# Kernel optimization log

Hardware: AMD Instinct MI355X
Metric: run time of the kernel (lower is better)

Reference implementation:

```python
import jax, jax.numpy as jnp
import numpy as np

N_NODES = 100000
N_EDGES = 800000
D_FEAT = 64
N_HIDDEN = 64
N_CLASSES = 16


def setup_inputs() -> dict:
    key = jax.random.key(0)
    ks = jax.random.split(key, 10)
    s = 1.0 / np.sqrt(N_HIDDEN)
    inp = {
        "x": jax.random.normal(ks[0], (N_NODES, D_FEAT), dtype=jnp.float32),
        "edge_index": jax.random.randint(ks[1], (2, N_EDGES), 0, N_NODES, dtype=jnp.int64)
        if jax.config.jax_enable_x64 else jax.random.randint(ks[1], (2, N_EDGES), 0, N_NODES, dtype=jnp.int32),
        "W1": jax.random.normal(ks[2], (D_FEAT, N_HIDDEN), dtype=jnp.float32) * s,
        "b1": jnp.zeros((N_HIDDEN,), jnp.float32),
        "W2": jax.random.normal(ks[3], (N_HIDDEN, N_HIDDEN), dtype=jnp.float32) * s,
        "b2": jnp.zeros((N_HIDDEN,), jnp.float32),
        "W3": jax.random.normal(ks[4], (N_HIDDEN, N_HIDDEN), dtype=jnp.float32) * s,
        "b3": jnp.zeros((N_HIDDEN,), jnp.float32),
        "Wf1": jax.random.normal(ks[5], (N_HIDDEN, N_HIDDEN), dtype=jnp.float32) * s,
        "bf1": jnp.zeros((N_HIDDEN,), jnp.float32),
        "Wf2": jax.random.normal(ks[6], (N_HIDDEN, N_HIDDEN), dtype=jnp.float32) * s,
        "bf2": jnp.zeros((N_HIDDEN,), jnp.float32),
        "Wf3": jax.random.normal(ks[7], (N_HIDDEN, N_CLASSES), dtype=jnp.float32) * s,
        "bf3": jnp.zeros((N_CLASSES,), jnp.float32),
    }
    return inp


def reference(x, edge_index, W1, b1, W2, b2, W3, b3, Wf1, bf1, Wf2, bf2, Wf3, bf3):
    N = x.shape[0]
    loops = jnp.arange(N, dtype=edge_index.dtype)
    src = jnp.concatenate([edge_index[0], loops])  # [E+N]
    dst = jnp.concatenate([edge_index[1], loops])
    # symmetric GCN normalization with self-loops (edge weight 1)
    deg = jax.ops.segment_sum(jnp.ones(src.shape[0], x.dtype), dst, num_segments=N)
    dis = jax.lax.rsqrt(jnp.maximum(deg, 1.0))  # deg >= 1 due to self-loops
    norm = dis[src] * dis[dst]  # [E+N]

    def gcn(h, W, b):
        h = h @ W  # [N, H]
        msg = h[src] * norm[:, None]  # [E+N, H] gather
        return jax.ops.segment_sum(msg, dst, num_segments=N) + b  # scatter-add

    y = jax.nn.relu(gcn(x, W1, b1))
    y = jax.nn.relu(gcn(y, W2, b2))
    y = jax.nn.relu(gcn(y, W3, b3))
    y = jax.nn.relu(y @ Wf1 + bf1)
    y = jax.nn.relu(y @ Wf2 + bf2)
    y = y @ Wf3 + bf3
    return jax.nn.log_softmax(y, axis=1)
```

## Files before the change

kernel.cpp:

```cpp
#include <hip/hip_runtime.h>
#include <hip/hip_bf16.h>

#define NN 100000
#define NE 800000
#define EBLK 391
#define NBUK 196
#define BSTRIDE 6144

typedef __attribute__((ext_vector_type(8))) short bf16x8;
typedef __attribute__((ext_vector_type(4))) float f32x4;

__device__ __forceinline__ unsigned short f2b(float f) {
  unsigned int x = __float_as_uint(f);
  return (unsigned short)((x + 0x7fffu + ((x >> 16) & 1u)) >> 16);
}
__device__ __forceinline__ float b2f(short us) {
  return __uint_as_float(((unsigned int)(unsigned short)us) << 16);
}
__device__ __forceinline__ void acc8(float* acc, bf16x8 v) {
#pragma unroll
  for (int i = 0; i < 8; ++i) acc[i] += b2f(v[i]);
}

static __global__ __launch_bounds__(256) void k_scatter(const int* __restrict__ src, const int* __restrict__ dst,
                                                        int* __restrict__ gcur, int* __restrict__ ebuf) {
  __shared__ int hist[256];
  __shared__ int lstart[256];
  __shared__ int gbase[256];
  __shared__ int cur[NBUK];
  __shared__ int2 sbuf[2048];
  int tid = threadIdx.x, blk = blockIdx.x;
  hist[tid] = 0;
  __syncthreads();
  int base = blk * 2048;
  int dd[8], ss[8];
#pragma unroll
  for (int i = 0; i < 8; ++i) {
    int e = base + tid + 256 * i;
    if (e < NE) {
      dd[i] = dst[e]; ss[i] = src[e];
      atomicAdd(&hist[dd[i] >> 9], 1);
    } else dd[i] = -1;
  }
  __syncthreads();
  int v = hist[tid];
  lstart[tid] = v;
  __syncthreads();
  for (int off = 1; off < 256; off <<= 1) {
    int t = (tid >= off) ? lstart[tid - off] : 0;
    __syncthreads();
    lstart[tid] += t;
    __syncthreads();
  }
  int excl = lstart[tid] - v;
  __syncthreads();
  lstart[tid] = excl;
  if (tid < NBUK) {
    cur[tid] = 0;
    gbase[tid] = (v > 0) ? atomicAdd(&gcur[tid], v) : 0;
  }
  __syncthreads();
#pragma unroll
  for (int i = 0; i < 8; ++i) {
    if (dd[i] >= 0) {
      int b = dd[i] >> 9;
      int p = atomicAdd(&cur[b], 1);
      sbuf[lstart[b] + p] = make_int2((ss[i] << 9) | (dd[i] & 511), b);
    }
  }
  __syncthreads();
  int m = NE - base; if (m > 2048) m = 2048;
#pragma unroll
  for (int i = 0; i < 8; ++i) {
    int j = tid + 256 * i;
    if (j < m) {
      int2 e = sbuf[j];
      int b = e.y;
      int gpos = b * BSTRIDE + gbase[b] + (j - lstart[b]);
      ebuf[gpos] = e.x;
    }
  }
}

static __global__ __launch_bounds__(256) void k_bucket(const int* __restrict__ ebuf, const int* __restrict__ gcur,
                                                       int2* __restrict__ rc, float* __restrict__ dis,
                                                       int* __restrict__ col_idx) {
  __shared__ int cnt[512];
  __shared__ int lrs[512];
  __shared__ int sd[256];
  int b = blockIdx.x, tid = threadIdx.x;
  int base_n = b << 9;
  int ebeg = b * BSTRIDE;
  int m = gcur[b];
  cnt[tid] = 0; cnt[tid + 256] = 0;
  __syncthreads();
  for (int j = tid; j < m; j += 256) atomicAdd(&cnt[ebuf[ebeg + j] & 511], 1);
  __syncthreads();
  int v0 = cnt[2 * tid], v1 = cnt[2 * tid + 1];
  int s = v0 + v1;
  sd[tid] = s;
  __syncthreads();
  for (int off = 1; off < 256; off <<= 1) {
    int t = (tid >= off) ? sd[tid - off] : 0;
    __syncthreads();
    sd[tid] += t;
    __syncthreads();
  }
  int excl = sd[tid] - s;
  lrs[2 * tid] = excl;
  lrs[2 * tid + 1] = excl + v0;
  __syncthreads();
  for (int i = tid; i < 512; i += 256) {
    int n = base_n + i;
    if (n < NN) {
      int c = cnt[i];
      rc[n] = make_int2(ebeg + lrs[i], c);
      dis[n] = 1.0f / sqrtf((float)c + 1.0f);
    }
  }
  for (int i = tid; i < 512; i += 256) cnt[i] = lrs[i];
  __syncthreads();
  for (int j = tid; j < m; j += 256) {
    int e = ebuf[ebeg + j];
    int p = atomicAdd(&cnt[e & 511], 1);
    col_idx[ebeg + p] = e >> 9;
  }
}

static __global__ __launch_bounds__(256) void k_wconv(
    const float* __restrict__ W1, const float* __restrict__ W2, const float* __restrict__ W3,
    const float* __restrict__ Wf1, const float* __restrict__ Wf2, const float* __restrict__ Wf3,
    short* __restrict__ W1t, short* __restrict__ W2t, short* __restrict__ W3t,
    short* __restrict__ Wf1t, short* __restrict__ Wf2t, short* __restrict__ Wf3t) {
  int b = blockIdx.x, tid = threadIdx.x;
  if (b < 5) {
    const float* W = (b == 0) ? W1 : (b == 1) ? W2 : (b == 2) ? W3 : (b == 3) ? Wf1 : Wf2;
    short* Wt = (b == 0) ? W1t : (b == 1) ? W2t : (b == 2) ? W3t : (b == 3) ? Wf1t : Wf2t;
#pragma unroll
    for (int i = 0; i < 16; ++i) {
      int idx = tid + 256 * i;
      int k = idx >> 6, nn = idx & 63;
      Wt[nn * 64 + k] = (short)f2b(W[idx]);
    }
  } else {
#pragma unroll
    for (int i = 0; i < 4; ++i) {
      int idx = tid + 256 * i;
      int k = idx >> 4, nn = idx & 15;
      Wf3t[nn * 64 + k] = (short)f2b(Wf3[idx]);
    }
  }
}

__device__ __forceinline__ bf16x8 load_a_frag_f32(const float* __restrict__ p, bool valid) {
  float4 f0 = valid ? *(const float4*)p : make_float4(0.f, 0.f, 0.f, 0.f);
  float4 f1 = valid ? *(const float4*)(p + 4) : make_float4(0.f, 0.f, 0.f, 0.f);
  bf16x8 a;
  a[0] = (short)f2b(f0.x); a[1] = (short)f2b(f0.y); a[2] = (short)f2b(f0.z); a[3] = (short)f2b(f0.w);
  a[4] = (short)f2b(f1.x); a[5] = (short)f2b(f1.y); a[6] = (short)f2b(f1.z); a[7] = (short)f2b(f1.w);
  return a;
}

__device__ __forceinline__ void mm_body(bf16x8 a0, bf16x8 a1, const short* __restrict__ Wt,
                                        const float* __restrict__ dis, short* __restrict__ out,
                                        int row0, int rlane, int g, int n) {
  f32x4 acc[4];
#pragma unroll
  for (int t = 0; t < 4; ++t) acc[t] = (f32x4){0.f, 0.f, 0.f, 0.f};
#pragma unroll
  for (int t = 0; t < 4; ++t) {
    bf16x8 b0 = *(const bf16x8*)(Wt + (rlane + 16 * t) * 64 + g * 8);
    bf16x8 b1 = *(const bf16x8*)(Wt + (rlane + 16 * t) * 64 + g * 8 + 32);
    acc[t] = __builtin_amdgcn_mfma_f32_16x16x32_bf16(a0, b0, acc[t], 0, 0, 0);
    acc[t] = __builtin_amdgcn_mfma_f32_16x16x32_bf16(a1, b1, acc[t], 0, 0, 0);
  }
#pragma unroll
  for (int r = 0; r < 4; ++r) {
    int gr = row0 + g * 4 + r;
    if (gr < n) {
      float s = dis[gr];
#pragma unroll
      for (int t = 0; t < 4; ++t)
        out[(size_t)gr * 64 + rlane + 16 * t] = (short)f2b(acc[t][r] * s);
    }
  }
}

static __global__ __launch_bounds__(256) void k_mm1(const float* __restrict__ in, const short* __restrict__ Wt,
                                                    const float* __restrict__ dis, short* __restrict__ out, int n) {
  int tid = threadIdx.x;
  int lane = tid & 63, w = tid >> 6;
  int row0 = blockIdx.x * 64 + w * 16;
  int rlane = lane & 15, g = lane >> 4;
  int arow = row0 + rlane;
  bool av = arow < n;
  const float* ap = in + (size_t)arow * 64 + g * 8;
  bf16x8 a0 = load_a_frag_f32(ap, av);
  bf16x8 a1 = load_a_frag_f32(ap + 32, av);
  mm_body(a0, a1, Wt, dis, out, row0, rlane, g, n);
}

__device__ __forceinline__ void agg_to_lds(const short* __restrict__ ht, const int2* __restrict__ rc,
                                           const int* __restrict__ col_idx, const float* __restrict__ dis,
                                           const float* __restrict__ bias, short (*Hsw)[72],
                                           int row0, int lane, int n) {
  int g = lane >> 3, f = lane & 7;
  float4 b0v = *(const float4*)&bias[f * 8];
  float4 b1v = *(const float4*)&bias[f * 8 + 4];
  float bb[8] = {b0v.x, b0v.y, b0v.z, b0v.w, b1v.x, b1v.y, b1v.z, b1v.w};
  int node0 = row0 + g, node1 = row0 + 8 + g;
  bool nv0 = node0 < n, nv1 = node1 < n;
  int2 rc0 = nv0 ? rc[node0] : make_int2(0, 0);
  int2 rc1 = nv1 ? rc[node1] : make_int2(0, 0);
  int beg0 = rc0.x, cnt0 = rc0.y;
  int beg1 = rc1.x, cnt1 = rc1.y;
  float dis0 = nv0 ? dis[node0] : 0.f;
  float dis1 = nv1 ? dis[node1] : 0.f;
  float acc0[8] = {0.f, 0.f, 0.f, 0.f, 0.f, 0.f, 0.f, 0.f};
  float acc1[8] = {0.f, 0.f, 0.f, 0.f, 0.f, 0.f, 0.f, 0.f};
  if (nv0) acc8(acc0, *(const bf16x8*)(ht + (size_t)node0 * 64 + f * 8));
  if (nv1) acc8(acc1, *(const bf16x8*)(ht + (size_t)node1 * 64 + f * 8));
  int cmax = max(cnt0, cnt1);
  for (int base = 0; base < cmax; base += 8) {
    int idx0 = (base + f < cnt0) ? col_idx[beg0 + base + f] : 0;
    int idx1 = (base + f < cnt1) ? col_idx[beg1 + base + f] : 0;
    int m0 = cnt0 - base; m0 = (m0 < 0) ? 0 : ((m0 > 8) ? 8 : m0);
    int m1 = cnt1 - base; m1 = (m1 < 0) ? 0 : ((m1 > 8) ? 8 : m1);
    int mm = (m0 > m1) ? m0 : m1;
    int e = 0;
    for (; e + 1 < mm; e += 2) {
      int s00 = __shfl(idx0, g * 8 + e);
      int s01 = __shfl(idx0, g * 8 + e + 1);
      int s10 = __shfl(idx1, g * 8 + e);
      int s11 = __shfl(idx1, g * 8 + e + 1);
      bf16x8 r00 = *(const bf16x8*)(ht + (size_t)s00 * 64 + f * 8);
      bf16x8 r10 = *(const bf16x8*)(ht + (size_t)s10 * 64 + f * 8);
      bf16x8 r01 = *(const bf16x8*)(ht + (size_t)s01 * 64 + f * 8);
      bf16x8 r11 = *(const bf16x8*)(ht + (size_t)s11 * 64 + f * 8);
      if (e < m0)     acc8(acc0, r00);
      if (e + 1 < m0) acc8(acc0, r01);
      if (e < m1)     acc8(acc1, r10);
      if (e + 1 < m1) acc8(acc1, r11);
    }
    if (e < mm) {
      int s00 = __shfl(idx0, g * 8 + e);
      int s10 = __shfl(idx1, g * 8 + e);
      bf16x8 r00 = *(const bf16x8*)(ht + (size_t)s00 * 64 + f * 8);
      bf16x8 r10 = *(const bf16x8*)(ht + (size_t)s10 * 64 + f * 8);
      if (e < m0) acc8(acc0, r00);
      if (e < m1) acc8(acc1, r10);
    }
  }
  bf16x8 o0, o1;
#pragma unroll
  for (int i = 0; i < 8; ++i) {
    o0[i] = (short)f2b(fmaxf(fmaf(dis0, acc0[i], bb[i]), 0.f));
    o1[i] = (short)f2b(fmaxf(fmaf(dis1, acc1[i], bb[i]), 0.f));
  }
  *(bf16x8*)&Hsw[g][f * 8] = o0;
  *(bf16x8*)&Hsw[8 + g][f * 8] = o1;
}

static __global__ __launch_bounds__(128) void k_aggmm(const short* __restrict__ ht, const int2* __restrict__ rc,
                                                      const int* __restrict__ col_idx, const float* __restrict__ dis,
                                                      const float* __restrict__ bias, const short* __restrict__ Wt,
                                                      short* __restrict__ out, int n) {
  __shared__ __align__(16) short Hs[2][16][72];
  int tid = threadIdx.x;
  int lane = tid & 63, w = tid >> 6;
  int row0 = blockIdx.x * 32 + w * 16;
  agg_to_lds(ht, rc, col_idx, dis, bias, Hs[w], row0, lane, n);
  int rlane = lane & 15, g = lane >> 4;
  bf16x8 a0 = *(const bf16x8*)&Hs[w][rlane][g * 8];
  bf16x8 a1 = *(const bf16x8*)&Hs[w][rlane][g * 8 + 32];
  mm_body(a0, a1, Wt, dis, out, row0, rlane, g, n);
}

static __global__ __launch_bounds__(128) void k_aggdense(const short* __restrict__ ht, const int2* __restrict__ rc,
    const int* __restrict__ col_idx, const float* __restrict__ dis, const float* __restrict__ bias,
    const short* __restrict__ W1t, const float* __restrict__ bf1,
    const short* __restrict__ W2t, const float* __restrict__ bf2,
    const short* __restrict__ W3t, const float* __restrict__ bf3,
    float* __restrict__ out, int n) {
  __shared__ __align__(16) short Hs[2][16][72];
  int tid = threadIdx.x;
  int lane = tid & 63, w = tid >> 6;
  int row0 = blockIdx.x * 32 + w * 16;
  agg_to_lds(ht, rc, col_idx, dis, bias, Hs[w], row0, lane, n);
  int rlane = lane & 15, g = lane >> 4;
  bf16x8 a0 = *(const bf16x8*)&Hs[w][rlane][g * 8];
  bf16x8 a1 = *(const bf16x8*)&Hs[w][rlane][g * 8 + 32];
  f32x4 acc[4];
#pragma unroll
  for (int t = 0; t < 4; ++t) acc[t] = (f32x4){0.f, 0.f, 0.f, 0.f};
#pragma unroll
  for (int t = 0; t < 4; ++t) {
    bf16x8 b0 = *(const bf16x8*)(W1t + (rlane + 16 * t) * 64 + g * 8);
    bf16x8 b1 = *(const bf16x8*)(W1t + (rlane + 16 * t) * 64 + g * 8 + 32);
    acc[t] = __builtin_amdgcn_mfma_f32_16x16x32_bf16(a0, b0, acc[t], 0, 0, 0);
    acc[t] = __builtin_amdgcn_mfma_f32_16x16x32_bf16(a1, b1, acc[t], 0, 0, 0);
  }
#pragma unroll
  for (int t = 0; t < 4; ++t) {
    float bb = bf1[16 * t + rlane];
#pragma unroll
    for (int r = 0; r < 4; ++r)
      Hs[w][g * 4 + r][16 * t + rlane] = (short)f2b(fmaxf(acc[t][r] + bb, 0.f));
  }
  bf16x8 c0 = *(const bf16x8*)&Hs[w][rlane][g * 8];
  bf16x8 c1 = *(const bf16x8*)&Hs[w][rlane][g * 8 + 32];
  f32x4 acc2[4];
#pragma unroll
  for (int t = 0; t < 4; ++t) acc2[t] = (f32x4){0.f, 0.f, 0.f, 0.f};
#pragma unroll
  for (int t = 0; t < 4; ++t) {
    bf16x8 b0 = *(const bf16x8*)(W2t + (rlane + 16 * t) * 64 + g * 8);
    bf16x8 b1 = *(const bf16x8*)(W2t + (rlane + 16 * t) * 64 + g * 8 + 32);
    acc2[t] = __builtin_amdgcn_mfma_f32_16x16x32_bf16(c0, b0, acc2[t], 0, 0, 0);
    acc2[t] = __builtin_amdgcn_mfma_f32_16x16x32_bf16(c1, b1, acc2[t], 0, 0, 0);
  }
#pragma unroll
  for (int t = 0; t < 4; ++t) {
    float bb = bf2[16 * t + rlane];
#pragma unroll
    for (int r = 0; r < 4; ++r)
      Hs[w][g * 4 + r][16 * t + rlane] = (short)f2b(fmaxf(acc2[t][r] + bb, 0.f));
  }
  bf16x8 d0 = *(const bf16x8*)&Hs[w][rlane][g * 8];
  bf16x8 d1 = *(const bf16x8*)&Hs[w][rlane][g * 8 + 32];
  bf16x8 e0 = *(const bf16x8*)(W3t + rlane * 64 + g * 8);
  bf16x8 e1 = *(const bf16x8*)(W3t + rlane * 64 + g * 8 + 32);
  f32x4 z = (f32x4){0.f, 0.f, 0.f, 0.f};
  z = __builtin_amdgcn_mfma_f32_16x16x32_bf16(d0, e0, z, 0, 0, 0);
  z = __builtin_amdgcn_mfma_f32_16x16x32_bf16(d1, e1, z, 0, 0, 0);
  float bsc = bf3[rlane];
#pragma unroll
  for (int r = 0; r < 4; ++r) {
    float zz = z[r] + bsc;
    float mx = zz;
    mx = fmaxf(mx, __shfl_xor(mx, 1));
    mx = fmaxf(mx, __shfl_xor(mx, 2));
    mx = fmaxf(mx, __shfl_xor(mx, 4));
    mx = fmaxf(mx, __shfl_xor(mx, 8));
    float ex = __expf(zz - mx);
    ex += __shfl_xor(ex, 1);
    ex += __shfl_xor(ex, 2);
    ex += __shfl_xor(ex, 4);
    ex += __shfl_xor(ex, 8);
    float lse = mx + __logf(ex);
    int gr = row0 + g * 4 + r;
    if (gr < n) out[(size_t)gr * 16 + rlane] = zz - lse;
  }
}

extern "C" void kernel_launch(void* const* d_in, const int* in_sizes, int n_in,
                              void* d_out, int out_size, void* d_ws, size_t ws_size,
                              hipStream_t stream) {
  (void)in_sizes; (void)n_in; (void)out_size; (void)ws_size;
  const float* x   = (const float*)d_in[0];
  const int*   ei  = (const int*)d_in[1];
  const float* W1  = (const float*)d_in[2];
  const float* b1  = (const float*)d_in[3];
  const float* W2  = (const float*)d_in[4];
  const float* b2  = (const float*)d_in[5];
  const float* W3  = (const float*)d_in[6];
  const float* b3  = (const float*)d_in[7];
  const float* Wf1 = (const float*)d_in[8];
  const float* bf1 = (const float*)d_in[9];
  const float* Wf2 = (const float*)d_in[10];
  const float* bf2 = (const float*)d_in[11];
  const float* Wf3 = (const float*)d_in[12];
  const float* bf3 = (const float*)d_in[13];
  float* outp = (float*)d_out;
  const int* srcp = ei;
  const int* dstp = ei + NE;

  char* ws = (char*)d_ws;
  size_t off = 0;
  auto alloc = [&](size_t bytes) { void* p = ws + off; off = (off + bytes + 255) & ~(size_t)255; return p; };
  int2*  rc     = (int2*)alloc((size_t)NN * 8);
  float* dis    = (float*)alloc((size_t)NN * 4);
  int*   gcur   = (int*)alloc(256 * 4);
  int*   colidx = (int*)alloc((size_t)NBUK * BSTRIDE * 4);
  short* W1t    = (short*)alloc(4096 * 2);
  short* W2t    = (short*)alloc(4096 * 2);
  short* W3t    = (short*)alloc(4096 * 2);
  short* Wf1t   = (short*)alloc(4096 * 2);
  short* Wf2t   = (short*)alloc(4096 * 2);
  short* Wf3t   = (short*)alloc(1024 * 2);
  short* bufA   = (short*)alloc((size_t)NN * 64 * 2);
  short* bufB   = (short*)alloc((size_t)NN * 64 * 2);
  int*   ebuf   = (int*)alloc((size_t)NBUK * BSTRIDE * 4);

  int gMM = (NN + 63) / 64;
  int gAG = (NN + 31) / 32;

  hipMemsetAsync(gcur, 0, 256 * 4, stream);
  k_wconv<<<6, 256, 0, stream>>>(W1, W2, W3, Wf1, Wf2, Wf3, W1t, W2t, W3t, Wf1t, Wf2t, Wf3t);
  k_scatter<<<EBLK, 256, 0, stream>>>(srcp, dstp, gcur, ebuf);
  k_bucket<<<NBUK, 256, 0, stream>>>(ebuf, gcur, rc, dis, colidx);

  k_mm1<<<gMM, 256, 0, stream>>>(x, W1t, dis, bufB, NN);
  k_aggmm<<<gAG, 128, 0, stream>>>(bufB, rc, colidx, dis, b1, W2t, bufA, NN);
  k_aggmm<<<gAG, 128, 0, stream>>>(bufA, rc, colidx, dis, b2, W3t, bufB, NN);
  k_aggdense<<<gAG, 128, 0, stream>>>(bufB, rc, colidx, dis, b3,
                                      Wf1t, bf1, Wf2t, bf2, Wf3t, bf3, outp, NN);
}
```

Measured before the change: 147.3 us.

## Fuse weight conversion into scatter kernel and regroup aggregation to one node per lane-group

The weight-conversion kernel is folded into the edge-scatter kernel as extra blocks, which removes one launch. The aggregation kernels now handle 16 nodes per block instead of 32. Each 8-lane group gathers a single node rather than interleaving two, and the two waves split the 64 output columns of the dense MFMA stage, synchronised through shared memory. The aim is more blocks and finer load balance for the irregular gather, at the cost of extra __syncthreads, less memory-level parallelism per lane, and an idle second wave in the final softmax stage.

Measured after the change: 137.7 us. 6.5% less time.

```diff
diff --git a/kernel.cpp b/kernel.cpp
--- a/kernel.cpp
+++ b/kernel.cpp
@@ -22,14 +22,39 @@
   for (int i = 0; i < 8; ++i) acc[i] += b2f(v[i]);
 }
 
-static __global__ __launch_bounds__(256) void k_scatter(const int* __restrict__ src, const int* __restrict__ dst,
-                                                        int* __restrict__ gcur, int* __restrict__ ebuf) {
+static __global__ __launch_bounds__(256) void k_scwc(const int* __restrict__ src, const int* __restrict__ dst,
+                                                     int* __restrict__ gcur, int* __restrict__ ebuf,
+    const float* __restrict__ W1, const float* __restrict__ W2, const float* __restrict__ W3,
+    const float* __restrict__ Wf1, const float* __restrict__ Wf2, const float* __restrict__ Wf3,
+    short* __restrict__ W1t, short* __restrict__ W2t, short* __restrict__ W3t,
+    short* __restrict__ Wf1t, short* __restrict__ Wf2t, short* __restrict__ Wf3t) {
+  int tid = threadIdx.x, blk = blockIdx.x;
+  if (blk >= EBLK) {
+    int b = blk - EBLK;
+    if (b < 5) {
+      const float* W = (b == 0) ? W1 : (b == 1) ? W2 : (b == 2) ? W3 : (b == 3) ? Wf1 : Wf2;
+      short* Wt = (b == 0) ? W1t : (b == 1) ? W2t : (b == 2) ? W3t : (b == 3) ? Wf1t : Wf2t;
+#pragma unroll
+      for (int i = 0; i < 16; ++i) {
+        int idx = tid + 256 * i;
+        int k = idx >> 6, nn = idx & 63;
+        Wt[nn * 64 + k] = (short)f2b(W[idx]);
+      }
+    } else {
+#pragma unroll
+      for (int i = 0; i < 4; ++i) {
+        int idx = tid + 256 * i;
+        int k = idx >> 4, nn = idx & 15;
+        Wf3t[nn * 64 + k] = (short)f2b(Wf3[idx]);
+      }
+    }
+    return;
+  }
   __shared__ int hist[256];
   __shared__ int lstart[256];
   __shared__ int gbase[256];
   __shared__ int cur[NBUK];
   __shared__ int2 sbuf[2048];
-  int tid = threadIdx.x, blk = blockIdx.x;
   hist[tid] = 0;
   __syncthreads();
   int base = blk * 2048;
@@ -124,31 +149,6 @@
     int e = ebuf[ebeg + j];
     int p = atomicAdd(&cnt[e & 511], 1);
     col_idx[ebeg + p] = e >> 9;
-  }
-}
-
-static __global__ __launch_bounds__(256) void k_wconv(
-    const float* __restrict__ W1, const float* __restrict__ W2, const float* __restrict__ W3,
-    const float* __restrict__ Wf1, const float* __restrict__ Wf2, const float* __restrict__ Wf3,
-    short* __restrict__ W1t, short* __restrict__ W2t, short* __restrict__ W3t,
-    short* __restrict__ Wf1t, short* __restrict__ Wf2t, short* __restrict__ Wf3t) {
-  int b = blockIdx.x, tid = threadIdx.x;
-  if (b < 5) {
-    const float* W = (b == 0) ? W1 : (b == 1) ? W2 : (b == 2) ? W3 : (b == 3) ? Wf1 : Wf2;
-    short* Wt = (b == 0) ? W1t : (b == 1) ? W2t : (b == 2) ? W3t : (b == 3) ? Wf1t : Wf2t;
-#pragma unroll
-    for (int i = 0; i < 16; ++i) {
-      int idx = tid + 256 * i;
-      int k = idx >> 6, nn = idx & 63;
-      Wt[nn * 64 + k] = (short)f2b(W[idx]);
-    }
-  } else {
-#pragma unroll
-    for (int i = 0; i < 4; ++i) {
-      int idx = tid + 256 * i;
-      int k = idx >> 4, nn = idx & 15;
-      Wf3t[nn * 64 + k] = (short)f2b(Wf3[idx]);
-    }
   }
 }
 
@@ -200,80 +200,71 @@
   mm_body(a0, a1, Wt, dis, out, row0, rlane, g, n);
 }
 
-__device__ __forceinline__ void agg_to_lds(const short* __restrict__ ht, const int2* __restrict__ rc,
-                                           const int* __restrict__ col_idx, const float* __restrict__ dis,
-                                           const float* __restrict__ bias, short (*Hsw)[72],
-                                           int row0, int lane, int n) {
+__device__ __forceinline__ void agg8_to_lds(const short* __restrict__ ht, const int2* __restrict__ rc,
+                                            const int* __restrict__ col_idx, const float* __restrict__ dis,
+                                            const float* __restrict__ bias, short (*Hs)[72],
+                                            int nodebase, int wrow0, int lane, int n) {
   int g = lane >> 3, f = lane & 7;
   float4 b0v = *(const float4*)&bias[f * 8];
   float4 b1v = *(const float4*)&bias[f * 8 + 4];
   float bb[8] = {b0v.x, b0v.y, b0v.z, b0v.w, b1v.x, b1v.y, b1v.z, b1v.w};
-  int node0 = row0 + g, node1 = row0 + 8 + g;
-  bool nv0 = node0 < n, nv1 = node1 < n;
-  int2 rc0 = nv0 ? rc[node0] : make_int2(0, 0);
-  int2 rc1 = nv1 ? rc[node1] : make_int2(0, 0);
-  int beg0 = rc0.x, cnt0 = rc0.y;
-  int beg1 = rc1.x, cnt1 = rc1.y;
-  float dis0 = nv0 ? dis[node0] : 0.f;
-  float dis1 = nv1 ? dis[node1] : 0.f;
-  float acc0[8] = {0.f, 0.f, 0.f, 0.f, 0.f, 0.f, 0.f, 0.f};
-  float acc1[8] = {0.f, 0.f, 0.f, 0.f, 0.f, 0.f, 0.f, 0.f};
-  if (nv0) acc8(acc0, *(const bf16x8*)(ht + (size_t)node0 * 64 + f * 8));
-  if (nv1) acc8(acc1, *(const bf16x8*)(ht + (size_t)node1 * 64 + f * 8));
-  int cmax = max(cnt0, cnt1);
-  for (int base = 0; base < cmax; base += 8) {
-    int idx0 = (base + f < cnt0) ? col_idx[beg0 + base + f] : 0;
-    int idx1 = (base + f < cnt1) ? col_idx[beg1 + base + f] : 0;
-    int m0 = cnt0 - base; m0 = (m0 < 0) ? 0 : ((m0 > 8) ? 8 : m0);
-    int m1 = cnt1 - base; m1 = (m1 < 0) ? 0 : ((m1 > 8) ? 8 : m1);
-    int mm = (m0 > m1) ? m0 : m1;
+  int node = nodebase + g;
+  bool nv = node < n;
+  int2 rcv = nv ? rc[node] : make_int2(0, 0);
+  int beg = rcv.x, cnt = rcv.y;
+  float ds = nv ? dis[node] : 0.f;
+  float acc[8] = {0.f, 0.f, 0.f, 0.f, 0.f, 0.f, 0.f, 0.f};
+  if (nv) acc8(acc, *(const bf16x8*)(ht + (size_t)node * 64 + f * 8));
+  for (int base = 0; base < cnt; base += 8) {
+    int mm = cnt - base; if (mm > 8) mm = 8;
+    int idx = (base + f < cnt) ? col_idx[beg + base + f] : 0;
     int e = 0;
     for (; e + 1 < mm; e += 2) {
-      int s00 = __shfl(idx0, g * 8 + e);
-      int s01 = __shfl(idx0, g * 8 + e + 1);
-      int s10 = __shfl(idx1, g * 8 + e);
-      int s11 = __shfl(idx1, g * 8 + e + 1);
-      bf16x8 r00 = *(const bf16x8*)(ht + (size_t)s00 * 64 + f * 8);
-      bf16x8 r10 = *(const bf16x8*)(ht + (size_t)s10 * 64 + f * 8);
-      bf16x8 r01 = *(const bf16x8*)(ht + (size_t)s01 * 64 + f * 8);
-      bf16x8 r11 = *(const bf16x8*)(ht + (size_t)s11 * 64 + f * 8);
-      if (e < m0)     acc8(acc0, r00);
-      if (e + 1 < m0) acc8(acc0, r01);
-      if (e < m1)     acc8(acc1, r10);
-      if (e + 1 < m1) acc8(acc1, r11);
+      int s0 = __shfl(idx, g * 8 + e);
+      int s1 = __shfl(idx, g * 8 + e + 1);
+      bf16x8 r0 = *(const bf16x8*)(ht + (size_t)s0 * 64 + f * 8);
+      bf16x8 r1 = *(const bf16x8*)(ht + (size_t)s1 * 64 + f * 8);
+      acc8(acc, r0); acc8(acc, r1);
     }
     if (e < mm) {
-      int s00 = __shfl(idx0, g * 8 + e);
-      int s10 = __shfl(idx1, g * 8 + e);
-      bf16x8 r00 = *(const bf16x8*)(ht + (size_t)s00 * 64 + f * 8);
-      bf16x8 r10 = *(const bf16x8*)(ht + (size_t)s10 * 64 + f * 8);
-      if (e < m0) acc8(acc0, r00);
-      if (e < m1) acc8(acc1, r10);
-    }
-  }
-  bf16x8 o0, o1;
-#pragma unroll
-  for (int i = 0; i < 8; ++i) {
-    o0[i] = (short)f2b(fmaxf(fmaf(dis0, acc0[i], bb[i]), 0.f));
-    o1[i] = (short)f2b(fmaxf(fmaf(dis1, acc1[i], bb[i]), 0.f));
-  }
-  *(bf16x8*)&Hsw[g][f * 8] = o0;
-  *(bf16x8*)&Hsw[8 + g][f * 8] = o1;
+      int s0 = __shfl(idx, g * 8 + e);
+      acc8(acc, *(const bf16x8*)(ht + (size_t)s0 * 64 + f * 8));
+    }
+  }
+  bf16x8 o;
+#pragma unroll
+  for (int i = 0; i < 8; ++i)
+    o[i] = (short)f2b(fmaxf(fmaf(ds, acc[i], bb[i]), 0.f));
+  *(bf16x8*)&Hs[wrow0 + g][f * 8] = o;
 }
 
 static __global__ __launch_bounds__(128) void k_aggmm(const short* __restrict__ ht, const int2* __restrict__ rc,
                                                       const int* __restrict__ col_idx, const float* __restrict__ dis,
                                                       const float* __restrict__ bias, const short* __restrict__ Wt,
                                                       short* __restrict__ out, int n) {
-  __shared__ __align__(16) short Hs[2][16][72];
+  __shared__ __align__(16) short Hs[16][72];
   int tid = threadIdx.x;
   int lane = tid & 63, w = tid >> 6;
-  int row0 = blockIdx.x * 32 + w * 16;
-  agg_to_lds(ht, rc, col_idx, dis, bias, Hs[w], row0, lane, n);
+  int row0 = blockIdx.x * 16;
+  agg8_to_lds(ht, rc, col_idx, dis, bias, Hs, row0 + w * 8, w * 8, lane, n);
+  __syncthreads();
   int rlane = lane & 15, g = lane >> 4;
-  bf16x8 a0 = *(const bf16x8*)&Hs[w][rlane][g * 8];
-  bf16x8 a1 = *(const bf16x8*)&Hs[w][rlane][g * 8 + 32];
-  mm_body(a0, a1, Wt, dis, out, row0, rlane, g, n);
+  bf16x8 a0 = *(const bf16x8*)&Hs[rlane][g * 8];
+  bf16x8 a1 = *(const bf16x8*)&Hs[rlane][g * 8 + 32];
+#pragma unroll
+  for (int tt = 0; tt < 2; ++tt) {
+    int t = 2 * w + tt;
+    bf16x8 b0 = *(const bf16x8*)(Wt + (rlane + 16 * t) * 64 + g * 8);
+    bf16x8 b1 = *(const bf16x8*)(Wt + (rlane + 16 * t) * 64 + g * 8 + 32);
+    f32x4 acc = (f32x4){0.f, 0.f, 0.f, 0.f};
+    acc = __builtin_amdgcn_mfma_f32_16x16x32_bf16(a0, b0, acc, 0, 0, 0);
+    acc = __builtin_amdgcn_mfma_f32_16x16x32_bf16(a1, b1, acc, 0, 0, 0);
+#pragma unroll
+    for (int r = 0; r < 4; ++r) {
+      int gr = row0 + g * 4 + r;
+      if (gr < n) out[(size_t)gr * 64 + rlane + 16 * t] = (short)f2b(acc[r] * dis[gr]);
+    }
+  }
 }
 
 static __global__ __launch_bounds__(128) void k_aggdense(const short* __restrict__ ht, const int2* __restrict__ rc,
@@ -282,74 +273,76 @@
     const short* __restrict__ W2t, const float* __restrict__ bf2,
     const short* __restrict__ W3t, const float* __restrict__ bf3,
     float* __restrict__ out, int n) {
-  __shared__ __align__(16) short Hs[2][16][72];
+  __shared__ __align__(16) short Hs[16][72];
+  __shared__ __align__(16) short H2[16][72];
   int tid = threadIdx.x;
   int lane = tid & 63, w = tid >> 6;
-  int row0 = blockIdx.x * 32 + w * 16;
-  agg_to_lds(ht, rc, col_idx, dis, bias, Hs[w], row0, lane, n);
+  int row0 = blockIdx.x * 16;
+  agg8_to_lds(ht, rc, col_idx, dis, bias, Hs, row0 + w * 8, w * 8, lane, n);
+  __syncthreads();
   int rlane = lane & 15, g = lane >> 4;
-  bf16x8 a0 = *(const bf16x8*)&Hs[w][rlane][g * 8];
-  bf16x8 a1 = *(const bf16x8*)&Hs[w][rlane][g * 8 + 32];
-  f32x4 acc[4];
-#pragma unroll
-  for (int t = 0; t < 4; ++t) acc[t] = (f32x4){0.f, 0.f, 0.f, 0.f};
-#pragma unroll
-  for (int t = 0; t < 4; ++t) {
-    bf16x8 b0 = *(const bf16x8*)(W1t + (rlane + 16 * t) * 64 + g * 8);
-    bf16x8 b1 = *(const bf16x8*)(W1t + (rlane + 16 * t) * 64 + g * 8 + 32);
-    acc[t] = __builtin_amdgcn_mfma_f32_16x16x32_bf16(a0, b0, acc[t], 0, 0, 0);
-    acc[t] = __builtin_amdgcn_mfma_f32_16x16x32_bf16(a1, b1, acc[t], 0, 0, 0);
-  }
-#pragma unroll
-  for (int t = 0; t < 4; ++t) {
-    float bb = bf1[16 * t + rlane];
-#pragma unroll
-    for (int r = 0; r < 4; ++r)
-      Hs[w][g * 4 + r][16 * t + rlane] = (short)f2b(fmaxf(acc[t][r] + bb, 0.f));
-  }
-  bf16x8 c0 = *(const bf16x8*)&Hs[w][rlane][g * 8];
-  bf16x8 c1 = *(const bf16x8*)&Hs[w][rlane][g * 8 + 32];
-  f32x4 acc2[4];
-#pragma unroll
-  for (int t = 0; t < 4; ++t) acc2[t] = (f32x4){0.f, 0.f, 0.f, 0.f};
-#pragma unroll
-  for (int t = 0; t < 4; ++t) {
-    bf16x8 b0 = *(const bf16x8*)(W2t + (rlane + 16 * t) * 64 + g * 8);
-    bf16x8 b1 = *(const bf16x8*)(W2t + (rlane + 16 * t) * 64 + g * 8 + 32);
-    acc2[t] = __builtin_amdgcn_mfma_f32_16x16x32_bf16(c0, b0, acc2[t], 0, 0, 0);
-    acc2[t] = __builtin_amdgcn_mfma_f32_16x16x32_bf16(c1, b1, acc2[t], 0, 0, 0);
-  }
-#pragma unroll
-  for (int t = 0; t < 4; ++t) {
-    float bb = bf2[16 * t + rlane];
-#pragma unroll
-    for (int r = 0; r < 4; ++r)
-      Hs[w][g * 4 + r][16 * t + rlane] = (short)f2b(fmaxf(acc2[t][r] + bb, 0.f));
-  }
-  bf16x8 d0 = *(const bf16x8*)&Hs[w][rlane][g * 8];
-  bf16x8 d1 = *(const bf16x8*)&Hs[w][rlane][g * 8 + 32];
-  bf16x8 e0 = *(const bf16x8*)(W3t + rlane * 64 + g * 8);
-  bf16x8 e1 = *(const bf16x8*)(W3t + rlane * 64 + g * 8 + 32);
-  f32x4 z = (f32x4){0.f, 0.f, 0.f, 0.f};
-  z = __builtin_amdgcn_mfma_f32_16x16x32_bf16(d0, e0, z, 0, 0, 0);
-  z = __builtin_amdgcn_mfma_f32_16x16x32_bf16(d1, e1, z, 0, 0, 0);
-  float bsc = bf3[rlane];
-#pragma unroll
-  for (int r = 0; r < 4; ++r) {
-    float zz = z[r] + bsc;
-    float mx = zz;
-    mx = fmaxf(mx, __shfl_xor(mx, 1));
-    mx = fmaxf(mx, __shfl_xor(mx, 2));
-    mx = fmaxf(mx, __shfl_xor(mx, 4));
-    mx = fmaxf(mx, __shfl_xor(mx, 8));
-    float ex = __expf(zz - mx);
-    ex += __shfl_xor(ex, 1);
-    ex += __shfl_xor(ex, 2);
-    ex += __shfl_xor(ex, 4);
-    ex += __shfl_xor(ex, 8);
-    float lse = mx + __logf(ex);
-    int gr = row0 + g * 4 + r;
-    if (gr < n) out[(size_t)gr * 16 + rlane] = zz - lse;
+  {
+    bf16x8 a0 = *(const bf16x8*)&Hs[rlane][g * 8];
+    bf16x8 a1 = *(const bf16x8*)&Hs[rlane][g * 8 + 32];
+#pragma unroll
+    for (int tt = 0; tt < 2; ++tt) {
+      int t = 2 * w + tt;
+      bf16x8 b0 = *(const bf16x8*)(W1t + (rlane + 16 * t) * 64 + g * 8);
+      bf16x8 b1 = *(const bf16x8*)(W1t + (rlane + 16 * t) * 64 + g * 8 + 32);
+      f32x4 acc = (f32x4){0.f, 0.f, 0.f, 0.f};
+      acc = __builtin_amdgcn_mfma_f32_16x16x32_bf16(a0, b0, acc, 0, 0, 0);
+      acc = __builtin_amdgcn_mfma_f32_16x16x32_bf16(a1, b1, acc, 0, 0, 0);
+      float bb = bf1[16 * t + rlane];
+#pragma unroll
+      for (int r = 0; r < 4; ++r)
+        H2[g * 4 + r][16 * t + rlane] = (short)f2b(fmaxf(acc[r] + bb, 0.f));
+    }
+  }
+  __syncthreads();
+  {
+    bf16x8 c0 = *(const bf16x8*)&H2[rlane][g * 8];
+    bf16x8 c1 = *(const bf16x8*)&H2[rlane][g * 8 + 32];
+#pragma unroll
+    for (int tt = 0; tt < 2; ++tt) {
+      int t = 2 * w + tt;
+      bf16x8 b0 = *(const bf16x8*)(W2t + (rlane + 16 * t) * 64 + g * 8);
+      bf16x8 b1 = *(const bf16x8*)(W2t + (rlane + 16 * t) * 64 + g * 8 + 32);
+      f32x4 acc = (f32x4){0.f, 0.f, 0.f, 0.f};
+      acc = __builtin_amdgcn_mfma_f32_16x16x32_bf16(c0, b0, acc, 0, 0, 0);
+      acc = __builtin_amdgcn_mfma_f32_16x16x32_bf16(c1, b1, acc, 0, 0, 0);
+      float bb = bf2[16 * t + rlane];
+#pragma unroll
+      for (int r = 0; r < 4; ++r)
+        Hs[g * 4 + r][16 * t + rlane] = (short)f2b(fmaxf(acc[r] + bb, 0.f));
+    }
+  }
+  __syncthreads();
+  if (w == 0) {
+    bf16x8 d0 = *(const bf16x8*)&Hs[rlane][g * 8];
+    bf16x8 d1 = *(const bf16x8*)&Hs[rlane][g * 8 + 32];
+    bf16x8 e0 = *(const bf16x8*)(W3t + rlane * 64 + g * 8);
+    bf16x8 e1 = *(const bf16x8*)(W3t + rlane * 64 + g * 8 + 32);
+    f32x4 z = (f32x4){0.f, 0.f, 0.f, 0.f};
+    z = __builtin_amdgcn_mfma_f32_16x16x32_bf16(d0, e0, z, 0, 0, 0);
+    z = __builtin_amdgcn_mfma_f32_16x16x32_bf16(d1, e1, z, 0, 0, 0);
+    float bsc = bf3[rlane];
+#pragma unroll
+    for (int r = 0; r < 4; ++r) {
+      float zz = z[r] + bsc;
+      float mx = zz;
+      mx = fmaxf(mx, __shfl_xor(mx, 1));
+      mx = fmaxf(mx, __shfl_xor(mx, 2));
+      mx = fmaxf(mx, __shfl_xor(mx, 4));
+      mx = fmaxf(mx, __shfl_xor(mx, 8));
+      float ex = __expf(zz - mx);
+      ex += __shfl_xor(ex, 1);
+      ex += __shfl_xor(ex, 2);
+      ex += __shfl_xor(ex, 4);
+      ex += __shfl_xor(ex, 8);
+      float lse = mx + __logf(ex);
+      int gr = row0 + g * 4 + r;
+      if (gr < n) out[(size_t)gr * 16 + rlane] = zz - lse;
+    }
   }
 }
 
@@ -393,11 +386,12 @@
   int*   ebuf   = (int*)alloc((size_t)NBUK * BSTRIDE * 4);
 
   int gMM = (NN + 63) / 64;
-  int gAG = (NN + 31) / 32;
+  int gAG = (NN + 15) / 16;
 
   hipMemsetAsync(gcur, 0, 256 * 4, stream);
-  k_wconv<<<6, 256, 0, stream>>>(W1, W2, W3, Wf1, Wf2, Wf3, W1t, W2t, W3t, Wf1t, Wf2t, Wf3t);
-  k_scatter<<<EBLK, 256, 0, stream>>>(srcp, dstp, gcur, ebuf);
+  k_scwc<<<EBLK + 6, 256, 0, stream>>>(srcp, dstp, gcur, ebuf,
+                                       W1, W2, W3, Wf1, Wf2, Wf3,
+                                       W1t, W2t, W3t, Wf1t, Wf2t, Wf3t);
   k_bucket<<<NBUK, 256, 0, stream>>>(ebuf, gcur, rc, dis, colidx);
 
   k_mm1<<<gMM, 256, 0, stream>>>(x, W1t, dis, bufB, NN);
```
